# Performance work log

Hardware: AMD Instinct MI355X
Metric: run time of the kernel (lower is better)

## Reference

```python
import jax, jax.numpy as jnp
import numpy as np

B, S, C = 8, 512, 1024
H = 16
R = 32            # lora_rank
LORA_ALPHA = 1.0  # lora scaling (alpha=1)
HID = C           # mlp_ratio = 1


def setup_inputs() -> dict:
    key = jax.random.key(0)
    ks = jax.random.split(key, 20)
    g = lambda k, shp, s=0.02: jax.random.normal(k, shp, dtype=jnp.float32) * s
    inp = {
        "x": jax.random.normal(ks[0], (B, S, C), dtype=jnp.float32),
        "mask": jax.random.randint(ks[1], (B, 3 * S), 0, 2).astype(bool),
        # qkv: Linear(dim, 3*dim, bias=False), stored [in, out]
        "qkv_w": g(ks[2], (C, 3 * C)),
        "qkv_la": g(ks[3], (C, R)),
        "qkv_lb": g(ks[4], (R, 3 * C)),
        "proj_w": g(ks[5], (C, C)),
        "proj_b": jnp.zeros((C,), jnp.float32),
        "proj_la": g(ks[6], (C, R)),
        "proj_lb": g(ks[7], (R, C)),
        "fc1_w": g(ks[8], (C, HID)),
        "fc1_b": jnp.zeros((HID,), jnp.float32),
        "fc1_la": g(ks[9], (C, R)),
        "fc1_lb": g(ks[10], (R, HID)),
        "fc2_w": g(ks[11], (HID, C)),
        "fc2_b": jnp.zeros((C,), jnp.float32),
        "fc2_la": g(ks[12], (C, R)),
        "fc2_lb": g(ks[13], (R, C)),
    }
    return inp


def reference(x, mask, qkv_w, qkv_la, qkv_lb, proj_w, proj_b, proj_la, proj_lb,
              fc1_w, fc1_b, fc1_la, fc1_lb, fc2_w, fc2_b, fc2_la, fc2_lb):
    # cross_modality='a', mask_modality='a' (constants)
    b, s, c = x.shape
    hd = c // H
    scale = hd ** (-0.5)

    # fused QKV + LoRA low-rank update
    qkv = x @ qkv_w + ((x @ qkv_la) @ qkv_lb) * LORA_ALPHA      # [B,S,3C]
    qkv = qkv.reshape(b, s, 3, H, hd).transpose(2, 0, 3, 1, 4)  # [3,B,H,S,hd]
    q, k, v = qkv[0] * scale, qkv[1], qkv[2]

    # fp32 QK^T, modality 'a' mask slice, fill -inf, softmax, NaN->0
    attn = jnp.einsum('bhqd,bhkd->bhqk',
                      q.astype(jnp.float32), k.astype(jnp.float32))
    m = mask[:, :s]                                             # 'a' slice
    attn = jnp.where(m[:, None, None, :], attn, -jnp.inf)
    attn = jax.nn.softmax(attn, axis=-1).astype(x.dtype)
    attn = jnp.where(jnp.isnan(attn), jnp.zeros((), x.dtype), attn)

    xo = jnp.einsum('bhqk,bhkd->bhqd', attn, v)                 # [B,H,S,hd]
    xo = xo.transpose(0, 2, 1, 3).reshape(b, s, c)

    # MLP (with LoRA on both fc layers); torch nn.GELU default = exact erf
    h = xo @ fc1_w + fc1_b + ((xo @ fc1_la) @ fc1_lb) * LORA_ALPHA
    h = jax.nn.gelu(h, approximate=False)
    h = h @ fc2_w + fc2_b + ((h @ fc2_la) @ fc2_lb) * LORA_ALPHA
    xo = xo + h

    out = xo @ proj_w + proj_b + ((xo @ proj_la) @ proj_lb) * LORA_ALPHA
    return out
```

## Files before the change

kernel.cpp:

```cpp
#include <hip/hip_runtime.h>

typedef _Float16 f16;
typedef _Float16 f16x8 __attribute__((ext_vector_type(8)));
typedef _Float16 f16x4v __attribute__((ext_vector_type(4)));
typedef float f32x4 __attribute__((ext_vector_type(4)));

#define DEVINL __device__ __forceinline__

DEVINL void gload16(const void* g, void* l) {
  __builtin_amdgcn_global_load_lds(
      (const __attribute__((address_space(1))) void*)g,
      (__attribute__((address_space(3))) void*)l, 16, 0, 0);
}

__global__ __launch_bounds__(256) void weff3(
    const float* __restrict__ W, const float* __restrict__ la,
    const float* __restrict__ lb, f16* __restrict__ WT,
    int N, int K, int scaleCols)
{
  __shared__ float La[64][36];
  __shared__ f16 Ts[64][72];
  int t = threadIdx.x;
  int n0 = blockIdx.x * 64, k0 = blockIdx.y * 64;
  int w = t >> 6, nn = t & 63;
  #pragma unroll
  for (int i = 0; i < 8; ++i) {
    int idx = i * 256 + t;
    int row = idx >> 5, r = idx & 31;
    La[row][r] = la[(size_t)(k0 + row) * 32 + r];
  }
  float lbr[32];
  #pragma unroll
  for (int r = 0; r < 32; ++r) lbr[r] = lb[(size_t)r * N + n0 + nn];
  float scale = (n0 + nn < scaleCols) ? 0.125f : 1.0f;
  __syncthreads();
  float prev = 0.0f;
  #pragma unroll
  for (int i = 0; i < 16; ++i) {
    int k = w * 16 + i;
    float acc = W[(size_t)(k0 + k) * N + n0 + nn];
    #pragma unroll
    for (int rc = 0; rc < 8; ++rc) {
      float4 a4 = *(const float4*)&La[k][rc * 4];
      acc += a4.x * lbr[rc * 4] + a4.y * lbr[rc * 4 + 1] +
             a4.z * lbr[rc * 4 + 2] + a4.w * lbr[rc * 4 + 3];
    }
    acc *= scale;
    if (i & 1) {
      union { f16 h[2]; unsigned u; } pk;
      pk.h[0] = (f16)prev; pk.h[1] = (f16)acc;
      *(unsigned*)&Ts[nn][k - 1] = pk.u;
    } else prev = acc;
  }
  __syncthreads();
  #pragma unroll
  for (int it = 0; it < 2; ++it) {
    int id = it * 256 + t;
    int row = id >> 3, c8 = id & 7;
    f16x8 h = *(const f16x8*)&Ts[row][c8 * 8];
    *(f16x8*)(WT + (size_t)(n0 + row) * K + k0 + c8 * 8) = h;
  }
}

__global__ __launch_bounds__(256) void cvt_f32_f16(const float* __restrict__ in,
                                                   f16* __restrict__ out)
{
  int i = (blockIdx.x * 256 + threadIdx.x) * 4;
  float4 v = *(const float4*)(in + i);
  f16x4v o = {(f16)v.x, (f16)v.y, (f16)v.z, (f16)v.w};
  *(f16x4v*)(out + i) = o;
}

__global__ __launch_bounds__(256) void mask_canon(const unsigned char* __restrict__ m,
                                                  unsigned char* __restrict__ out)
{
  __shared__ int flag;
  if (threadIdx.x == 0) flag = 0;
  __syncthreads();
  int found = 0;
  for (int p = threadIdx.x; p < 12288; p += 256)
    if ((p & 3) && m[p]) found = 1;
  if (found) flag = 1;
  __syncthreads();
  int u8 = flag;
  const int* mi = (const int*)m;
  for (int idx = threadIdx.x; idx < 4096; idx += 256) {
    int b = idx >> 9, k = idx & 511;
    int v = u8 ? (int)m[b * 1536 + k] : mi[b * 1536 + k];
    out[idx] = (unsigned char)(v != 0);
  }
}

template <int EPI, int BM>
__global__ __launch_bounds__(256, 3) void gemmk(
    const f16* __restrict__ A, const f16* __restrict__ Bt,
    int M, int N, int K,
    const float* __restrict__ bias, const f16* __restrict__ resid,
    f16* __restrict__ outH, float* __restrict__ outF,
    f16* __restrict__ Qo, f16* __restrict__ Ko, f16* __restrict__ Vto)
{
  constexpr int MF = BM / 32;
  __shared__ __align__(16) f16 As[2][BM * 32];
  __shared__ __align__(16) f16 Bs[2][128 * 32];
  int tid = threadIdx.x, wid = tid >> 6, l = tid & 63;
  int lg = l >> 4, lr = l & 15;
  int nbx = gridDim.x;
  int flat = blockIdx.y * nbx + blockIdx.x;
  int xcd = flat & 7, idx = flat >> 3;
  int mc = nbx >> 3;
  int bm = (xcd * mc + idx % mc) * BM;
  int bn = (idx / mc) * 128;
  int wr = (wid >> 1) * (BM / 2), wc = (wid & 1) * 64;
  f32x4 acc[MF][4] = {};

  int swz = ((l & 3) ^ ((l >> 3) & 3)) * 8;
  const f16* gA = A + (size_t)(bm + wid * (BM / 4) + (l >> 2)) * K + swz;
  const f16* gB = Bt + (size_t)(bn + wid * 32 + (l >> 2)) * K + swz;
  int xr = (lr >> 1) & 3;

  #pragma unroll
  for (int ig = 0; ig < BM / 64; ++ig)
    gload16(gA + (size_t)(ig * 16) * K, As[0] + (wid * (BM / 4) + ig * 16) * 32);
  #pragma unroll
  for (int ig = 0; ig < 2; ++ig)
    gload16(gB + (size_t)(ig * 16) * K, Bs[0] + (wid * 32 + ig * 16) * 32);
  __syncthreads();

  int nt = K >> 5;
  for (int ts = 0; ts < nt; ++ts) {
    int cur = ts & 1, nxt = cur ^ 1;
    if (ts + 1 < nt) {
      int k1 = (ts + 1) << 5;
      #pragma unroll
      for (int ig = 0; ig < BM / 64; ++ig)
        gload16(gA + (size_t)(ig * 16) * K + k1, As[nxt] + (wid * (BM / 4) + ig * 16) * 32);
      #pragma unroll
      for (int ig = 0; ig < 2; ++ig)
        gload16(gB + (size_t)(ig * 16) * K + k1, Bs[nxt] + (wid * 32 + ig * 16) * 32);
    }
    const f16* Ac = As[cur];
    const f16* Bc = Bs[cur];
    f16x8 bf[4];
    #pragma unroll
    for (int j = 0; j < 4; ++j) {
      int row = wc + j * 16 + lr;
      bf[j] = *(const f16x8*)(Bc + row * 32 + ((lg ^ xr) * 8));
    }
    __builtin_amdgcn_s_setprio(1);
    #pragma unroll
    for (int i = 0; i < MF; ++i) {
      int row = wr + i * 16 + lr;
      f16x8 af = *(const f16x8*)(Ac + row * 32 + ((lg ^ xr) * 8));
      #pragma unroll
      for (int j = 0; j < 4; ++j)
        acc[i][j] = __builtin_amdgcn_mfma_f32_16x16x32_f16(af, bf[j], acc[i][j], 0, 0, 0);
    }
    __builtin_amdgcn_s_setprio(0);
    __syncthreads();
  }

  #pragma unroll
  for (int i = 0; i < MF; ++i) {
    #pragma unroll
    for (int j = 0; j < 4; ++j) {
      int n = bn + wc + j * 16 + lr;
      float bv = (EPI >= 1) ? bias[n] : 0.0f;
      #pragma unroll
      for (int r = 0; r < 4; ++r) {
        int m = bm + wr + i * 16 + lg * 4 + r;
        float v = acc[i][j][r];
        if (EPI == 0) {
          int bb = m >> 9, ss = m & 511;
          int which = n >> 10, c = n & 1023, hh = c >> 6, dd = c & 63;
          size_t base = (size_t)(bb * 16 + hh);
          if (which == 0)      Qo[(base * 512 + ss) * 64 + dd] = (f16)v;
          else if (which == 1) Ko[(base * 512 + ss) * 64 + dd] = (f16)v;
          else                 Vto[(base * 64 + dd) * 512 + ss] = (f16)v;
        } else if (EPI == 1) {
          v += bv;
          v = 0.5f * v * (1.0f + erff(v * 0.70710678118654752f));
          outH[(size_t)m * N + n] = (f16)v;
        } else if (EPI == 2) {
          v += bv + (float)resid[(size_t)m * N + n];
          outH[(size_t)m * N + n] = (f16)v;
        } else {
          outF[(size_t)m * N + n] = v + bv;
        }
      }
    }
  }
}

__global__ __launch_bounds__(256, 2) void attn_kernel(
    const f16* __restrict__ Q, const f16* __restrict__ Kc,
    const f16* __restrict__ Vt, const unsigned char* __restrict__ cmask,
    f16* __restrict__ XO)
{
  __shared__ __align__(16) f16 Ks[128 * 64];
  __shared__ __align__(16) f16 Vs[64 * 128];
  __shared__ __align__(16) f16 Ps[4 * 32 * 128];
  int tid = threadIdx.x, w = tid >> 6, l = tid & 63;
  int lg = l >> 4, lr = l & 15;
  int flat = blockIdx.y * 4 + blockIdx.x;
  flat = (flat & 7) * 64 + (flat >> 3);
  int qblk = flat & 3, bh = flat >> 2;
  int b = bh >> 4, h = bh & 15;
  const f16* Qg = Q + (size_t)bh * 512 * 64 + qblk * 128 * 64;
  const f16* Kg = Kc + (size_t)bh * 512 * 64;
  const f16* Vg = Vt + (size_t)bh * 64 * 512;
  const unsigned char* mb = cmask + b * 512;

  f16x8 qf[2][2];
  #pragma unroll
  for (int i = 0; i < 2; ++i)
    #pragma unroll
    for (int kc = 0; kc < 2; ++kc)
      qf[i][kc] = *(const f16x8*)(Qg + (size_t)(w * 32 + i * 16 + lr) * 64 + kc * 32 + lg * 8);

  f32x4 O[2][4] = {};
  float mrow[2][4], lrow[2][4];
  #pragma unroll
  for (int i = 0; i < 2; ++i)
    #pragma unroll
    for (int r = 0; r < 4; ++r) { mrow[i][r] = -1e30f; lrow[i][r] = 0.0f; }

  f16* Pw = Ps + w * 32 * 128;

  int kR = tid >> 3, kC = (tid & 7) * 8;
  int vR = tid >> 4, vC = (tid & 15) * 8;
  f16x8 kreg[4], vreg[4];
  #pragma unroll
  for (int i = 0; i < 4; ++i) {
    kreg[i] = *(const f16x8*)(Kg + (size_t)(i * 32 + kR) * 64 + kC);
    vreg[i] = *(const f16x8*)(Vg + (size_t)(i * 16 + vR) * 512 + vC);
  }

  for (int kt = 0; kt < 4; ++kt) {
    #pragma unroll
    for (int i = 0; i < 4; ++i) {
      int krow = i * 32 + kR;
      *(f16x8*)(Ks + krow * 64 + (((tid & 7) ^ (krow & 7)) * 8)) = kreg[i];
      int vrow = i * 16 + vR;
      *(f16x8*)(Vs + vrow * 128 + (((tid & 15) ^ (vrow & 7)) * 8)) = vreg[i];
    }
    __syncthreads();
    if (kt < 3) {
      #pragma unroll
      for (int i = 0; i < 4; ++i) {
        kreg[i] = *(const f16x8*)(Kg + (size_t)((kt + 1) * 128 + i * 32 + kR) * 64 + kC);
        vreg[i] = *(const f16x8*)(Vg + (size_t)(i * 16 + vR) * 512 + (kt + 1) * 128 + vC);
      }
    }

    int x = lr & 7;
    f32x4 sc[2][8] = {};
    __builtin_amdgcn_s_setprio(1);
    #pragma unroll
    for (int j = 0; j < 8; ++j) {
      const f16* krow = Ks + (j * 16 + lr) * 64;
      f16x8 kf0 = *(const f16x8*)(krow + ((lg ^ x) * 8));
      f16x8 kf1 = *(const f16x8*)(krow + (((4 + lg) ^ x) * 8));
      sc[0][j] = __builtin_amdgcn_mfma_f32_16x16x32_f16(qf[0][0], kf0, sc[0][j], 0, 0, 0);
      sc[0][j] = __builtin_amdgcn_mfma_f32_16x16x32_f16(qf[0][1], kf1, sc[0][j], 0, 0, 0);
      sc[1][j] = __builtin_amdgcn_mfma_f32_16x16x32_f16(qf[1][0], kf0, sc[1][j], 0, 0, 0);
      sc[1][j] = __builtin_amdgcn_mfma_f32_16x16x32_f16(qf[1][1], kf1, sc[1][j], 0, 0, 0);
    }
    __builtin_amdgcn_s_setprio(0);
    bool keep[8];
    #pragma unroll
    for (int j = 0; j < 8; ++j) keep[j] = mb[kt * 128 + j * 16 + lr] != 0;
    #pragma unroll
    for (int i = 0; i < 2; ++i)
      #pragma unroll
      for (int j = 0; j < 8; ++j)
        #pragma unroll
        for (int r = 0; r < 4; ++r)
          sc[i][j][r] = keep[j] ? sc[i][j][r] : -1e30f;

    #pragma unroll
    for (int i = 0; i < 2; ++i) {
      #pragma unroll
      for (int r = 0; r < 4; ++r) {
        float pm = sc[i][0][r];
        #pragma unroll
        for (int j = 1; j < 8; ++j) pm = fmaxf(pm, sc[i][j][r]);
        pm = fmaxf(pm, __shfl_xor(pm, 1));
        pm = fmaxf(pm, __shfl_xor(pm, 2));
        pm = fmaxf(pm, __shfl_xor(pm, 4));
        pm = fmaxf(pm, __shfl_xor(pm, 8));
        float mn = fmaxf(mrow[i][r], pm);
        float alpha = __expf(mrow[i][r] - mn);
        mrow[i][r] = mn;
        lrow[i][r] *= alpha;
        #pragma unroll
        for (int jd = 0; jd < 4; ++jd) O[i][jd][r] *= alpha;
      }
    }
    #pragma unroll
    for (int i = 0; i < 2; ++i) {
      float rs[4] = {0.f, 0.f, 0.f, 0.f};
      #pragma unroll
      for (int j = 0; j < 8; ++j)
        #pragma unroll
        for (int r = 0; r < 4; ++r) {
          float p = __expf(sc[i][j][r] - mrow[i][r]);
          rs[r] += p;
          int prow = i * 16 + lg * 4 + r;
          int pc = j * 16 + lr;
          Pw[prow * 128 + ((((pc >> 3) ^ (prow & 7)) << 3) | (pc & 7))] = (f16)p;
        }
      #pragma unroll
      for (int r = 0; r < 4; ++r) {
        float s = rs[r];
        s += __shfl_xor(s, 1); s += __shfl_xor(s, 2);
        s += __shfl_xor(s, 4); s += __shfl_xor(s, 8);
        lrow[i][r] += s;
      }
    }
    __builtin_amdgcn_s_setprio(1);
    #pragma unroll
    for (int kk = 0; kk < 4; ++kk) {
      int c0 = ((kk * 4 + lg) ^ x) * 8;
      f16x8 pa0 = *(const f16x8*)(Pw + lr * 128 + c0);
      f16x8 pa1 = *(const f16x8*)(Pw + (16 + lr) * 128 + c0);
      #pragma unroll
      for (int jd = 0; jd < 4; ++jd) {
        f16x8 vb = *(const f16x8*)(Vs + (jd * 16 + lr) * 128 + c0);
        O[0][jd] = __builtin_amdgcn_mfma_f32_16x16x32_f16(pa0, vb, O[0][jd], 0, 0, 0);
        O[1][jd] = __builtin_amdgcn_mfma_f32_16x16x32_f16(pa1, vb, O[1][jd], 0, 0, 0);
      }
    }
    __builtin_amdgcn_s_setprio(0);
    __syncthreads();
  }

  #pragma unroll
  for (int i = 0; i < 2; ++i)
    #pragma unroll
    for (int r = 0; r < 4; ++r) {
      int q = qblk * 128 + w * 32 + i * 16 + lg * 4 + r;
      float inv = 1.0f / lrow[i][r];
      #pragma unroll
      for (int jd = 0; jd < 4; ++jd) {
        int c = h * 64 + jd * 16 + lr;
        XO[((size_t)b * 512 + q) * 1024 + c] = (f16)(O[i][jd][r] * inv);
      }
    }
}

extern "C" void kernel_launch(void* const* d_in, const int* in_sizes, int n_in,
                              void* d_out, int out_size, void* d_ws, size_t ws_size,
                              hipStream_t stream)
{
  (void)in_sizes; (void)n_in; (void)out_size; (void)ws_size;
  const float* x            = (const float*)d_in[0];
  const unsigned char* mask = (const unsigned char*)d_in[1];
  const float* qkv_w   = (const float*)d_in[2];
  const float* qkv_la  = (const float*)d_in[3];
  const float* qkv_lb  = (const float*)d_in[4];
  const float* proj_w  = (const float*)d_in[5];
  const float* proj_b  = (const float*)d_in[6];
  const float* proj_la = (const float*)d_in[7];
  const float* proj_lb = (const float*)d_in[8];
  const float* fc1_w   = (const float*)d_in[9];
  const float* fc1_b   = (const float*)d_in[10];
  const float* fc1_la  = (const float*)d_in[11];
  const float* fc1_lb  = (const float*)d_in[12];
  const float* fc2_w   = (const float*)d_in[13];
  const float* fc2_b   = (const float*)d_in[14];
  const float* fc2_la  = (const float*)d_in[15];
  const float* fc2_lb  = (const float*)d_in[16];
  float* out = (float*)d_out;

  f16* p = (f16*)d_ws;
  f16* WqkvT = p; p += 3072 * 1024;
  f16* W1T   = p; p += 1024 * 1024;
  f16* W2T   = p; p += 1024 * 1024;
  f16* WpT   = p; p += 1024 * 1024;
  f16* Xh    = p; p += 4096 * 1024;
  f16* Qb    = p; p += 128 * 512 * 64;
  f16* Kb    = p; p += 128 * 512 * 64;
  f16* Vt    = p; p += 128 * 64 * 512;
  f16* XO    = p; p += 4096 * 1024;
  unsigned char* cmask = (unsigned char*)p;
  f16* Hb  = Qb;
  f16* XO2 = Xh;

  weff3<<<dim3(48, 16), 256, 0, stream>>>(qkv_w, qkv_la, qkv_lb, WqkvT, 3072, 1024, 1024);
  weff3<<<dim3(16, 16), 256, 0, stream>>>(fc1_w, fc1_la, fc1_lb, W1T, 1024, 1024, 0);
  weff3<<<dim3(16, 16), 256, 0, stream>>>(fc2_w, fc2_la, fc2_lb, W2T, 1024, 1024, 0);
  weff3<<<dim3(16, 16), 256, 0, stream>>>(proj_w, proj_la, proj_lb, WpT, 1024, 1024, 0);
  cvt_f32_f16<<<4096, 256, 0, stream>>>(x, Xh);
  mask_canon<<<1, 256, 0, stream>>>(mask, cmask);

  gemmk<0, 128><<<dim3(32, 24), 256, 0, stream>>>(Xh, WqkvT, 4096, 3072, 1024,
      nullptr, nullptr, nullptr, nullptr, Qb, Kb, Vt);
  attn_kernel<<<dim3(4, 128), 256, 0, stream>>>(Qb, Kb, Vt, cmask, XO);
  gemmk<1, 64><<<dim3(64, 8), 256, 0, stream>>>(XO, W1T, 4096, 1024, 1024,
      fc1_b, nullptr, Hb, nullptr, nullptr, nullptr, nullptr);
  gemmk<2, 64><<<dim3(64, 8), 256, 0, stream>>>(Hb, W2T, 4096, 1024, 1024,
      fc2_b, XO, XO2, nullptr, nullptr, nullptr, nullptr);
  gemmk<3, 64><<<dim3(64, 8), 256, 0, stream>>>(XO2, WpT, 4096, 1024, 1024,
      proj_b, nullptr, nullptr, out, nullptr, nullptr, nullptr);
}
```

Baseline: 283.0 us.

## Use triple-buffered LDS pipeline with fine-grained vmcnt waits in GEMM

Rewrites the GEMM main loop to keep three LDS stages in flight, prefetching two K-tiles ahead. Explicit s_waitcnt vmcnt counts replace the full syncthreads so load latency can overlap MFMA work. It also fixes the M tile at 128 for every GEMM, which halves the grid for the 1024-wide layers (256 blocks). The cost is more LDS per block, which may reduce occupancy, and fewer blocks on the small GEMMs.

```diff
diff --git a/kernel.cpp b/kernel.cpp
--- a/kernel.cpp
+++ b/kernel.cpp
@@ -91,7 +91,7 @@
   }
 }
 
-template <int EPI, int BM>
+template <int EPI>
 __global__ __launch_bounds__(256, 3) void gemmk(
     const f16* __restrict__ A, const f16* __restrict__ Bt,
     int M, int N, int K,
@@ -99,68 +99,79 @@
     f16* __restrict__ outH, float* __restrict__ outF,
     f16* __restrict__ Qo, f16* __restrict__ Ko, f16* __restrict__ Vto)
 {
-  constexpr int MF = BM / 32;
-  __shared__ __align__(16) f16 As[2][BM * 32];
-  __shared__ __align__(16) f16 Bs[2][128 * 32];
+  __shared__ __align__(16) f16 As[3][128 * 32];
+  __shared__ __align__(16) f16 Bs[3][128 * 32];
   int tid = threadIdx.x, wid = tid >> 6, l = tid & 63;
   int lg = l >> 4, lr = l & 15;
   int nbx = gridDim.x;
   int flat = blockIdx.y * nbx + blockIdx.x;
   int xcd = flat & 7, idx = flat >> 3;
   int mc = nbx >> 3;
-  int bm = (xcd * mc + idx % mc) * BM;
+  int bm = (xcd * mc + idx % mc) * 128;
   int bn = (idx / mc) * 128;
-  int wr = (wid >> 1) * (BM / 2), wc = (wid & 1) * 64;
-  f32x4 acc[MF][4] = {};
+  int wr = (wid >> 1) * 64, wc = (wid & 1) * 64;
+  f32x4 acc[4][4] = {};
 
   int swz = ((l & 3) ^ ((l >> 3) & 3)) * 8;
-  const f16* gA = A + (size_t)(bm + wid * (BM / 4) + (l >> 2)) * K + swz;
+  const f16* gA = A + (size_t)(bm + wid * 32 + (l >> 2)) * K + swz;
   const f16* gB = Bt + (size_t)(bn + wid * 32 + (l >> 2)) * K + swz;
+  int lofs = wid * 32 * 32;
   int xr = (lr >> 1) & 3;
 
-  #pragma unroll
-  for (int ig = 0; ig < BM / 64; ++ig)
-    gload16(gA + (size_t)(ig * 16) * K, As[0] + (wid * (BM / 4) + ig * 16) * 32);
-  #pragma unroll
-  for (int ig = 0; ig < 2; ++ig)
-    gload16(gB + (size_t)(ig * 16) * K, Bs[0] + (wid * 32 + ig * 16) * 32);
-  __syncthreads();
+  f16* A0 = As[0]; f16* A1 = As[1]; f16* A2 = As[2];
+  f16* B0 = Bs[0]; f16* B1 = Bs[1]; f16* B2 = Bs[2];
+
+  #pragma unroll
+  for (int ig = 0; ig < 2; ++ig) {
+    gload16(gA + (size_t)(ig * 16) * K, A0 + lofs + ig * 16 * 32);
+    gload16(gB + (size_t)(ig * 16) * K, B0 + lofs + ig * 16 * 32);
+  }
+  #pragma unroll
+  for (int ig = 0; ig < 2; ++ig) {
+    gload16(gA + (size_t)(ig * 16) * K + 32, A1 + lofs + ig * 16 * 32);
+    gload16(gB + (size_t)(ig * 16) * K + 32, B1 + lofs + ig * 16 * 32);
+  }
 
   int nt = K >> 5;
-  for (int ts = 0; ts < nt; ++ts) {
-    int cur = ts & 1, nxt = cur ^ 1;
-    if (ts + 1 < nt) {
-      int k1 = (ts + 1) << 5;
-      #pragma unroll
-      for (int ig = 0; ig < BM / 64; ++ig)
-        gload16(gA + (size_t)(ig * 16) * K + k1, As[nxt] + (wid * (BM / 4) + ig * 16) * 32);
-      #pragma unroll
-      for (int ig = 0; ig < 2; ++ig)
-        gload16(gB + (size_t)(ig * 16) * K + k1, Bs[nxt] + (wid * 32 + ig * 16) * 32);
-    }
-    const f16* Ac = As[cur];
-    const f16* Bc = Bs[cur];
-    f16x8 bf[4];
-    #pragma unroll
-    for (int j = 0; j < 4; ++j) {
-      int row = wc + j * 16 + lr;
-      bf[j] = *(const f16x8*)(Bc + row * 32 + ((lg ^ xr) * 8));
-    }
+  for (int t = 0; t < nt; ++t) {
+    if (t + 2 < nt) {
+      int k2 = (t + 2) << 5;
+      #pragma unroll
+      for (int ig = 0; ig < 2; ++ig) {
+        gload16(gA + (size_t)(ig * 16) * K + k2, A2 + lofs + ig * 16 * 32);
+        gload16(gB + (size_t)(ig * 16) * K + k2, B2 + lofs + ig * 16 * 32);
+      }
+      asm volatile("s_waitcnt vmcnt(8)" ::: "memory");
+    } else if (t + 2 == nt) {
+      asm volatile("s_waitcnt vmcnt(4)" ::: "memory");
+    } else {
+      asm volatile("s_waitcnt vmcnt(0)" ::: "memory");
+    }
+    __builtin_amdgcn_s_barrier();
+
+    f16x8 af[4], bf[4];
+    #pragma unroll
+    for (int i = 0; i < 4; ++i)
+      af[i] = *(const f16x8*)(A0 + (wr + i * 16 + lr) * 32 + ((lg ^ xr) * 8));
+    #pragma unroll
+    for (int j = 0; j < 4; ++j)
+      bf[j] = *(const f16x8*)(B0 + (wc + j * 16 + lr) * 32 + ((lg ^ xr) * 8));
     __builtin_amdgcn_s_setprio(1);
     #pragma unroll
-    for (int i = 0; i < MF; ++i) {
-      int row = wr + i * 16 + lr;
-      f16x8 af = *(const f16x8*)(Ac + row * 32 + ((lg ^ xr) * 8));
+    for (int i = 0; i < 4; ++i)
       #pragma unroll
       for (int j = 0; j < 4; ++j)
-        acc[i][j] = __builtin_amdgcn_mfma_f32_16x16x32_f16(af, bf[j], acc[i][j], 0, 0, 0);
-    }
+        acc[i][j] = __builtin_amdgcn_mfma_f32_16x16x32_f16(af[i], bf[j], acc[i][j], 0, 0, 0);
     __builtin_amdgcn_s_setprio(0);
-    __syncthreads();
-  }
-
-  #pragma unroll
-  for (int i = 0; i < MF; ++i) {
+    __builtin_amdgcn_sched_barrier(0);
+    __builtin_amdgcn_s_barrier();
+
+    f16* tA = A0; A0 = A1; A1 = A2; A2 = tA;
+    f16* tB = B0; B0 = B1; B1 = B2; B2 = tB;
+  }
+
+  #pragma unroll
+  for (int i = 0; i < 4; ++i) {
     #pragma unroll
     for (int j = 0; j < 4; ++j) {
       int n = bn + wc + j * 16 + lr;
@@ -393,13 +404,13 @@
   cvt_f32_f16<<<4096, 256, 0, stream>>>(x, Xh);
   mask_canon<<<1, 256, 0, stream>>>(mask, cmask);
 
-  gemmk<0, 128><<<dim3(32, 24), 256, 0, stream>>>(Xh, WqkvT, 4096, 3072, 1024,
+  gemmk<0><<<dim3(32, 24), 256, 0, stream>>>(Xh, WqkvT, 4096, 3072, 1024,
       nullptr, nullptr, nullptr, nullptr, Qb, Kb, Vt);
   attn_kernel<<<dim3(4, 128), 256, 0, stream>>>(Qb, Kb, Vt, cmask, XO);
-  gemmk<1, 64><<<dim3(64, 8), 256, 0, stream>>>(XO, W1T, 4096, 1024, 1024,
+  gemmk<1><<<dim3(32, 8), 256, 0, stream>>>(XO, W1T, 4096, 1024, 1024,
       fc1_b, nullptr, Hb, nullptr, nullptr, nullptr, nullptr);
-  gemmk<2, 64><<<dim3(64, 8), 256, 0, stream>>>(Hb, W2T, 4096, 1024, 1024,
+  gemmk<2><<<dim3(32, 8), 256, 0, stream>>>(Hb, W2T, 4096, 1024, 1024,
       fc2_b, XO, XO2, nullptr, nullptr, nullptr, nullptr);
-  gemmk<3, 64><<<dim3(64, 8), 256, 0, stream>>>(XO2, WpT, 4096, 1024, 1024,
+  gemmk<3><<<dim3(32, 8), 256, 0, stream>>>(XO2, WpT, 4096, 1024, 1024,
       proj_b, nullptr, nullptr, out, nullptr, nullptr, nullptr);
 }
```

Measured after the change: 293.4 us. 3.7% more time.
